# Kernel tuning notes

Hardware: AMD Instinct MI355X
Metric: run time of the kernel (lower is better)

The kernel has to match this reference:

```python
import jax, jax.numpy as jnp
import numpy as np

B, NPTS = 2, 60000
NX, NY = 256, 256
PCR0, PCR1 = -32.0, -32.0
PS0, PS1 = 0.25, 0.25
MAXPP = 32      # max points per pillar
MAXP = 12000    # max pillars
C = 64          # lidar_channels
SENT = NX * NY  # sentinel pillar id (> any valid id)
NEG = -1e9
EPS = 1e-5


def setup_inputs():
    key = jax.random.key(0)
    ks = jax.random.split(key, 16)
    xy = jax.random.uniform(ks[0], (B, NPTS, 2), minval=-34.0, maxval=34.0)
    z = jax.random.uniform(ks[1], (B, NPTS, 1), minval=-3.0, maxval=1.0)
    ir = jax.random.uniform(ks[2], (B, NPTS, 2))
    pts = jnp.concatenate([xy, z, ir], axis=-1).astype(jnp.float32)
    mask = jax.random.uniform(ks[3], (B, NPTS)) < 0.98

    def lin(k, i, o):
        return (jax.random.normal(k, (i, o)) / np.sqrt(i)).astype(jnp.float32)

    inp = {"lidar_points": pts, "lidar_mask": mask,
           "w1": lin(ks[4], 10, 64), "b1": 0.01 * jax.random.normal(ks[5], (64,), jnp.float32),
           "g1": jnp.ones(64, jnp.float32), "be1": jnp.zeros(64, jnp.float32),
           "w2": lin(ks[6], 64, 64), "b2": 0.01 * jax.random.normal(ks[7], (64,), jnp.float32),
           "g2": jnp.ones(64, jnp.float32), "be2": jnp.zeros(64, jnp.float32)}
    for i, n in enumerate(["1", "2", "3"]):
        inp["cw" + n] = (jax.random.normal(ks[8 + i], (64, 64, 3, 3)) / np.sqrt(64 * 9)).astype(jnp.float32)
        inp["cb" + n] = 0.01 * jax.random.normal(ks[11 + i], (64,), jnp.float32)
        inp["cg" + n] = jnp.ones(64, jnp.float32)
        inp["cbe" + n] = jnp.zeros(64, jnp.float32)
    return inp


def bn1d(x, g, b):  # training-mode BN over rows (biased var), matches torch BatchNorm1d forward
    m = x.mean(0)
    v = ((x - m) ** 2).mean(0)
    return (x - m) * jax.lax.rsqrt(v + EPS) * g + b


def bn2d(x, g, b):  # training-mode BN over (N,H,W) per channel
    m = x.mean((0, 2, 3), keepdims=True)
    v = ((x - m) ** 2).mean((0, 2, 3), keepdims=True)
    return (x - m) * jax.lax.rsqrt(v + EPS) * g[None, :, None, None] + b[None, :, None, None]


def conv3(x, w, b):
    y = jax.lax.conv_general_dilated(x, w, (1, 1), 'SAME',
                                     dimension_numbers=('NCHW', 'OIHW', 'NCHW'))
    return y + b[None, :, None, None]


def pillarize(pts, msk):
    """pts: (N,5) xyzir, msk: (N,) bool -> padded pillar tensors (fixed shapes)."""
    n = pts.shape[0]
    ix = jnp.clip(((pts[:, 0] - PCR0) / PS0).astype(jnp.int32), 0, NX - 1)
    iy = jnp.clip(((pts[:, 1] - PCR1) / PS1).astype(jnp.int32), 0, NY - 1)
    pid = jnp.where(msk, iy * NX + ix, SENT)
    # sorted unique ids; keep the first (smallest) MAXP, like torch.unique + truncation
    spid = jnp.sort(pid)
    is_new = jnp.concatenate([jnp.array([True]), spid[1:] != spid[:-1]])
    urank = jnp.cumsum(is_new) - 1
    dest = jnp.where(is_new & (urank < MAXP) & (spid < SENT), urank, MAXP)
    uids = jnp.full((MAXP + 1,), SENT, dtype=pid.dtype).at[dest].set(spid)[:MAXP]  # ascending, SENT-padded
    inv = jnp.clip(jnp.searchsorted(uids, pid), 0, MAXP - 1)
    valid = (uids[inv] == pid) & (pid < SENT)
    # rank of each point within its pillar, in original point order (stable sort)
    seg = jnp.where(valid, inv, MAXP)
    order = jnp.argsort(seg)  # stable
    sseg = seg[order]
    pos = jnp.arange(n)
    first = jnp.concatenate([jnp.array([True]), sseg[1:] != sseg[:-1]])
    start = jax.lax.cummax(jnp.where(first, pos, 0))
    rank = jnp.zeros(n, jnp.int32).at[order].set((pos - start).astype(jnp.int32))
    keep = valid & (rank < MAXPP)  # first MAXPP points per pillar (matches truncation-then-mean)
    seg2 = jnp.where(keep, inv, MAXP)  # dump slot = MAXP
    cnt = jnp.zeros(MAXP + 1, pts.dtype).at[seg2].add(1.0)
    sums = jnp.zeros((MAXP + 1, 3), pts.dtype).at[seg2].add(jnp.where(keep[:, None], pts[:, :3], 0.0))
    mean = sums / jnp.maximum(cnt, 1.0)[:, None]
    ctr = mean[seg2]  # per-point pillar centroid (over kept points)
    gx = PCR0 + ((pid % NX).astype(pts.dtype) + 0.5) * PS0
    gy = PCR1 + ((pid // NX).astype(pts.dtype) + 0.5) * PS1
    aug = jnp.concatenate([pts, pts[:, :3] - ctr, gx[:, None], gy[:, None]], axis=1)  # (N,10)
    rk = jnp.minimum(rank, MAXPP - 1)
    pf = jnp.zeros((MAXP + 1, MAXPP, 10), pts.dtype).at[seg2, rk].set(
        jnp.where(keep[:, None], aug, 0.0))[:MAXP]
    pm = jnp.zeros((MAXP + 1, MAXPP), bool).at[seg2, rk].set(keep)[:MAXP]
    pvalid = uids < SENT
    coords = jnp.where(pvalid[:, None], jnp.stack([uids % NX, uids // NX], axis=-1), 0)
    return pf, pm, coords, pvalid


def pillar_net(pf, pm, w1, b1, g1, be1, w2, b2, g2, be2):
    npil, pp, ci = pf.shape
    x = pf.reshape(npil * pp, ci) @ w1 + b1
    x = jax.nn.relu(bn1d(x, g1, be1))
    x = x @ w2 + b2
    x = jax.nn.relu(bn1d(x, g2, be2))
    x = x.reshape(npil, pp, -1)
    x = jnp.where(pm[:, :, None], x, NEG)
    return x.max(axis=1)  # (npil, C)


def reference(lidar_points, lidar_mask, w1, b1, g1, be1, w2, b2, g2, be2,
              cw1, cb1, cg1, cbe1, cw2, cb2, cg2, cbe2, cw3, cb3, cg3, cbe3):
    pf, pm, coords, pvalid = jax.vmap(pillarize)(lidar_points, lidar_mask)
    # pillar net is applied per batch element in the original loop -> per-sample BN stats
    feat = jax.vmap(lambda a, m: pillar_net(a, m, w1, b1, g1, be1, w2, b2, g2, be2))(pf, pm)
    lin = coords[..., 1] * NX + coords[..., 0]          # (B, MAXP)
    f = jnp.where(pvalid[..., None], feat, 0.0)          # padded pillars contribute nothing
    bev = jax.vmap(lambda l, ff: jnp.zeros((NY * NX, C), ff.dtype).at[l].add(ff))(lin, f)
    bev = bev.reshape(-1, NY, NX, C).transpose(0, 3, 1, 2)  # (B,C,NY,NX)
    x = jax.nn.relu(bn2d(conv3(bev, cw1, cb1), cg1, cbe1))
    x = jax.nn.relu(bn2d(conv3(x, cw2, cb2), cg2, cbe2))
    x = jax.nn.relu(bn2d(conv3(x, cw3, cb3), cg3, cbe3))
    return x
```

## Files before the change

kernel.cpp:

```cpp
#include <hip/hip_runtime.h>

#define NPTS 60000
#define NXG 256
#define NCELL 65536
#define MAXP 12000
#define MAXPP 32
#define NROWS (MAXP*MAXPP)

typedef float f32x32 __attribute__((ext_vector_type(32)));
typedef float f32x4  __attribute__((ext_vector_type(4)));
typedef short s16x8  __attribute__((ext_vector_type(8)));

__device__ __forceinline__ short to_bf16(float f){
  unsigned u = __float_as_uint(f);
  unsigned r = (u + 0x7FFFu + ((u>>16)&1u)) >> 16;
  return (short)r;
}

__global__ void probe_mask(const unsigned* __restrict__ m, int* __restrict__ misc){
  __shared__ int cf32, cbig;
  if (threadIdx.x==0){ cf32=0; cbig=0; }
  __syncthreads();
  int lf=0, lb=0;
  for (int k=0;k<4;k++){
    unsigned x = m[threadIdx.x*4+k];
    if (x==0x3f800000u) lf++;
    else if (x>1u) lb++;
  }
  atomicAdd(&cf32, lf); atomicAdd(&cbig, lb);
  __syncthreads();
  if (threadIdx.x==0){
    int mode=0;
    if (cf32>64) mode=2; else if (cbig>0) mode=1;
    misc[0]=mode;
  }
}

__global__ void compute_pid(const float* __restrict__ pts, const void* __restrict__ maskp,
                            const int* __restrict__ misc, int* __restrict__ pid,
                            int* __restrict__ ccnt){
  int i = blockIdx.x*blockDim.x + threadIdx.x;
  if (i>=NPTS) return;
  int b = blockIdx.y;
  int gi = b*NPTS+i;
  int mode = misc[0];
  bool m;
  if (mode==0)      m = ((const int*)maskp)[gi]!=0;
  else if (mode==1) m = ((const unsigned char*)maskp)[gi]!=0;
  else              m = ((const float*)maskp)[gi]!=0.f;
  int cell = -1;
  if (m){
    float x = pts[(size_t)gi*5+0], y = pts[(size_t)gi*5+1];
    int ix = (int)((x - (-32.0f)) / 0.25f);
    ix = ix<0?0:(ix>255?255:ix);
    int iy = (int)((y - (-32.0f)) / 0.25f);
    iy = iy<0?0:(iy>255?255:iy);
    cell = iy*NXG + ix;
    atomicAdd(&ccnt[b*NCELL+cell], 1);
  }
  pid[gi] = cell;
}

__global__ __launch_bounds__(256) void scan_a(const int* __restrict__ ccnt,
                                              int2* __restrict__ bpart){
  int b = blockIdx.y, blk = blockIdx.x, t = threadIdx.x;
  int4 v = *(const int4*)&ccnt[b*NCELL + blk*1024 + t*4];
  int occ = (v.x>0)+(v.y>0)+(v.z>0)+(v.w>0);
  int cnt = v.x+v.y+v.z+v.w;
  #pragma unroll
  for (int off=32; off>0; off>>=1){
    occ += __shfl_xor(occ, off, 64);
    cnt += __shfl_xor(cnt, off, 64);
  }
  __shared__ int so[4], sc[4];
  int wv = t>>6, lane = t&63;
  if (lane==0){ so[wv]=occ; sc[wv]=cnt; }
  __syncthreads();
  if (t==0) bpart[b*64+blk] = make_int2(so[0]+so[1]+so[2]+so[3], sc[0]+sc[1]+sc[2]+sc[3]);
}

__global__ __launch_bounds__(256) void scan_b(const int* __restrict__ ccnt,
    const int2* __restrict__ bpart,
    int* __restrict__ crank, int* __restrict__ cstart, int* __restrict__ pcell,
    int* __restrict__ misc, int* __restrict__ heavy){
  __shared__ int swo[4], swc[4], sk[4];
  __shared__ int bo_, bc_;
  int b = blockIdx.y, blk = blockIdx.x, t = threadIdx.x;
  int wv = t>>6, lane = t&63;
  if (t < 64){
    int2 p = bpart[b*64+t];
    int po = (t<blk)? p.x : 0;
    int pc = (t<blk)? p.y : 0;
    int to = p.x;
    int tc = p.y;
    #pragma unroll
    for (int off=32; off>0; off>>=1){
      po += __shfl_xor(po, off, 64);
      pc += __shfl_xor(pc, off, 64);
      to += __shfl_xor(to, off, 64);
      tc += __shfl_xor(tc, off, 64);
    }
    if (t==0){
      bo_ = po; bc_ = pc;
      if (blk==0){
        misc[1+b] = (to < MAXP) ? to : MAXP;
        misc[5+b] = tc;
      }
    }
  }
  int4 v = *(const int4*)&ccnt[b*NCELL + blk*1024 + t*4];
  int occ = (v.x>0)+(v.y>0)+(v.z>0)+(v.w>0);
  int cnt = v.x+v.y+v.z+v.w;
  int io = occ, ic = cnt;
  #pragma unroll
  for (int off=1; off<64; off<<=1){
    int ao = __shfl_up(io, off, 64);
    int ac = __shfl_up(ic, off, 64);
    if (lane >= off){ io += ao; ic += ac; }
  }
  if (lane==63){ swo[wv]=io; swc[wv]=ic; }
  __syncthreads();
  int wvo=0, wvc=0;
  #pragma unroll
  for (int w2=0; w2<4; w2++){
    if (w2<wv){ wvo += swo[w2]; wvc += swc[w2]; }
  }
  int eo = bo_ + wvo + io - occ;
  int ec = bc_ + wvc + ic - cnt;
  int kept = 0;
  int cellb = blk*1024 + t*4;
  int vv[4] = {v.x,v.y,v.z,v.w};
  #pragma unroll
  for (int j=0;j<4;j++){
    int c = cellb+j; int val = vv[j];
    if (val>0){
      crank[b*NCELL+c]=eo; cstart[b*NCELL+c]=ec;
      if (eo<MAXP){
        pcell[b*MAXP+eo]=c;
        kept += (val<MAXPP)? val : MAXPP;
        if (val>MAXPP){
          int hi = atomicAdd(&heavy[b],1);
          if (hi<64) heavy[2 + b*64 + hi] = c;
        }
      }
      eo++; ec+=val;
    }
  }
  #pragma unroll
  for (int off=32; off>0; off>>=1) kept += __shfl_xor(kept, off, 64);
  if (lane==0) sk[wv]=kept;
  __syncthreads();
  if (t==0) atomicAdd(&misc[3+b], sk[0]+sk[1]+sk[2]+sk[3]);
}

__global__ void scatter_points(const int* __restrict__ pid, const int* __restrict__ ccnt,
    const int* __restrict__ crank, const int* __restrict__ cstart,
    int* __restrict__ ctmp, int* __restrict__ plist, int* __restrict__ pptr){
  int i = blockIdx.x*blockDim.x + threadIdx.x;
  if (i>=NPTS) return;
  int b = blockIdx.y;
  int gi = b*NPTS+i;
  int cell = pid[gi];
  if (cell<0) return;
  int bc = b*NCELL+cell;
  int pos = cstart[bc] + atomicAdd(&ctmp[bc],1);
  plist[b*NPTS+pos] = i;
  int r = crank[bc];
  if (r>=0 && r<MAXP && ccnt[bc]<=MAXPP) pptr[gi] = r;
}

__global__ void heavy_select(const int* __restrict__ ccnt, const int* __restrict__ crank,
    const int* __restrict__ cstart, const int* __restrict__ plist,
    const int* __restrict__ heavy, int* __restrict__ pptr){
  int b = blockIdx.y;
  int hn = heavy[b]; if (hn>64) hn=64;
  if ((int)blockIdx.x >= hn) return;
  int cell = heavy[2 + b*64 + blockIdx.x];
  int bc = b*NCELL+cell;
  int cnt = ccnt[bc], start = cstart[bc], pr = crank[bc];
  for (int e=threadIdx.x; e<cnt; e+=blockDim.x){
    int pe = plist[b*NPTS+start+e];
    int rank=0;
    for (int k=0;k<cnt;k++) rank += (plist[b*NPTS+start+k] < pe);
    if (rank<MAXPP) pptr[b*NPTS+pe] = pr;
  }
}

__global__ __launch_bounds__(256) void gather_cpts(const float* __restrict__ pts,
    const int* __restrict__ pid, const int* __restrict__ pptr,
    const int* __restrict__ plist, const int* __restrict__ misc,
    float* __restrict__ cpts, float* __restrict__ psum){
  int pos = blockIdx.x*256 + threadIdx.x;
  int b = blockIdx.y;
  if (pos >= misc[5+b]) return;
  int i = plist[b*NPTS+pos];
  int gi = b*NPTS+i;
  const float* qp = &pts[(size_t)gi*5];
  float x=qp[0], y=qp[1], z=qp[2], i1=qp[3], i2=qp[4];
  int cell = pid[gi];
  int rid = pptr[gi];
  float gx = -32.0f + ((float)(cell&255)+0.5f)*0.25f;
  float gy = -32.0f + ((float)(cell>>8)+0.5f)*0.25f;
  float4* cp = (float4*)&cpts[(size_t)(b*NPTS+pos)*8];
  cp[0] = make_float4(x,y,z,i1);
  cp[1] = make_float4(i2,gx,gy,__int_as_float(rid));
  if (rid>=0){
    float* s = &psum[(size_t)(b*MAXP+rid)*4];
    atomicAdd(s+0,x); atomicAdd(s+1,y); atomicAdd(s+2,z); atomicAdd(s+3,1.f);
  }
}

__global__ void centroid_fin(float* __restrict__ psum){
  int i = blockIdx.x*blockDim.x + threadIdx.x;
  if (i>=2*MAXP) return;
  float* s = &psum[(size_t)i*4];
  float inv = 1.0f / fmaxf(s[3],1.0f);
  s[0]*=inv; s[1]*=inv; s[2]*=inv;
}

#define MM_ACC(K,V) { if ((K)<32) m0[(K)&31]+=(V); else if ((K)<64) m1[((K)-32)&31]+=(V); else m2+=(V); }
__global__ __launch_bounds__(256) void moments(const float* __restrict__ cpts,
    const float* __restrict__ psum, const int* __restrict__ misc,
    float* __restrict__ lstat){
  int b = blockIdx.y;
  int n = misc[5+b];
  f32x32 m0, m1; float m2 = 0.f;
  #pragma unroll
  for (int j=0;j<32;j++){ m0[j]=0.f; m1[j]=0.f; }
  for (int pos = blockIdx.x*256+threadIdx.x; pos<n; pos += gridDim.x*256){
    const float4* cp = (const float4*)&cpts[(size_t)(b*NPTS+pos)*8];
    float4 f1 = cp[0], f2 = cp[1];
    int rid = __float_as_int(f2.w);
    if (rid<0) continue;
    float4 mc = *(const float4*)&psum[(size_t)(b*MAXP+rid)*4];
    float aug[10] = {f1.x,f1.y,f1.z,f1.w,f2.x,
                     f1.x-mc.x, f1.y-mc.y, f1.z-mc.z, f2.y, f2.z};
    #pragma unroll
    for (int d=0; d<10; d++){
      #pragma unroll
      for (int e=d; e<10; e++){
        const int k = d*10 - d*(d-1)/2 + (e-d);
        MM_ACC(k, aug[d]*aug[e]);
      }
      const int kl = 55+d;
      MM_ACC(kl, aug[d]);
    }
  }
  int lane = threadIdx.x & 63;
  int rep = ((blockIdx.x*256+threadIdx.x)>>6) & 15;
  float* dst = &lstat[(size_t)(rep*2+b)*65];
  #pragma unroll
  for (int j=0;j<32;j++){
    float v = m0[j];
    #pragma unroll
    for (int off=32; off>0; off>>=1) v += __shfl_xor(v, off, 64);
    if (lane==0) atomicAdd(&dst[j], v);
  }
  #pragma unroll
  for (int j=0;j<32;j++){
    float v = m1[j];
    #pragma unroll
    for (int off=32; off>0; off>>=1) v += __shfl_xor(v, off, 64);
    if (lane==0) atomicAdd(&dst[32+j], v);
  }
  {
    float v = m2;
    #pragma unroll
    for (int off=32; off>0; off>>=1) v += __shfl_xor(v, off, 64);
    if (lane==0) atomicAdd(&dst[64], v);
  }
}

__global__ void stats_fin1(const float* __restrict__ w1, const float* __restrict__ b1,
    const float* __restrict__ g1, const float* __restrict__ be1,
    const float* __restrict__ w2, const float* __restrict__ b2,
    const float* __restrict__ lstat, float* __restrict__ stats,
    const int* __restrict__ misc){
  __shared__ float M[65];
  __shared__ float z0s[64];
  int b = blockIdx.x, c = threadIdx.x;
  for (int e=c; e<65; e+=64){
    float s=0.f;
    for (int r=0;r<16;r++) s += lstat[(size_t)(r*2+b)*65+e];
    M[e]=s;
  }
  __syncthreads();
  float* S = &stats[(size_t)b*512];
  float wcol[10];
  #pragma unroll
  for (int d=0;d<10;d++) wcol[d] = w1[d*64+c];
  float b1c = b1[c];
  float nk = (float)misc[3+b];
  const float N = (float)NROWS;
  float pad = N - nk;
  float lw = 0.f;
  #pragma unroll
  for (int d=0;d<10;d++) lw += M[55+d]*wcol[d];
  float s = nk*b1c + lw;
  float qq = nk*b1c*b1c + 2.f*b1c*lw;
  #pragma unroll
  for (int d=0; d<10; d++){
    #pragma unroll
    for (int e=d; e<10; e++){
      float m = M[d*10 - d*(d-1)/2 + (e-d)];
      qq += ((d==e)?1.f:2.f)*m*wcol[d]*wcol[e];
    }
  }
  float St = s + pad*b1c;
  float Qt = qq + pad*b1c*b1c;
  float mu = St/N;
  float var = fmaxf(Qt/N - mu*mu, 0.f);
  float sc = g1[c]*rsqrtf(var+1e-5f);
  float sh = be1[c]-mu*sc;
  S[256+c]=sc; S[320+c]=sh;
  float z0 = fmaxf(b1c*sc+sh, 0.f);
  z0s[c]=z0;
  __syncthreads();
  float t0 = b2[c];
  for (int i2=0;i2<64;i2++) t0 += z0s[i2]*w2[(size_t)i2*64+c];
  S[128+c]=pad*t0; S[192+c]=pad*t0*t0;
}

__global__ __launch_bounds__(256) void pillar_mlp(const float* __restrict__ cpts,
    const int* __restrict__ pcell, const int* __restrict__ cstart,
    const int* __restrict__ ccnt, const float* __restrict__ psum,
    const int* __restrict__ misc,
    const float* __restrict__ w1, const float* __restrict__ b1,
    const float* __restrict__ w2, const float* __restrict__ b2,
    const float* __restrict__ stats, float* __restrict__ l2stat,
    float* __restrict__ fmx, float* __restrict__ fmn){
  const int lane = threadIdx.x & 63;
  float w1c[10];
  #pragma unroll
  for (int d=0;d<10;d++) w1c[d] = w1[d*64+lane];
  f32x32 w2lo, w2hi;
  #pragma unroll
  for (int c=0;c<32;c++) w2lo[c] = w2[(size_t)c*64+lane];
  #pragma unroll
  for (int c=0;c<32;c++) w2hi[c] = w2[(size_t)(c+32)*64+lane];
  const float b1c = b1[lane], b2c = b2[lane];
  const float sc1_0 = stats[256+lane], sh1_0 = stats[320+lane];
  const float sc1_1 = stats[512+256+lane], sh1_1 = stats[512+320+lane];
  const int npil0 = misc[1], npil1 = misc[2];
  float s2_0=0.f, q2_0=0.f, s2_1=0.f, q2_1=0.f;

  const int wglobal = (blockIdx.x*256 + threadIdx.x) >> 6;
  const int nwaves = (gridDim.x*256) >> 6;
  for (int qq = wglobal; qq < 2*MAXP; qq += nwaves){
    int b = (qq >= MAXP) ? 1 : 0;
    int p = qq - b*MAXP;
    int npil = b ? npil1 : npil0;
    if (p >= npil) continue;
    int cell = pcell[b*MAXP+p];
    int bc = b*NCELL+cell;
    int cnt = ccnt[bc], start = cstart[bc];
    const float* mc = &psum[(size_t)(b*MAXP+p)*4];
    float mx = mc[0], my = mc[1], mz = mc[2];
    float gx = -32.0f + ((float)(cell&255)+0.5f)*0.25f;
    float gy = -32.0f + ((float)(cell>>8)+0.5f)*0.25f;
    float sc1 = b ? sc1_1 : sc1_0;
    float sh1 = b ? sh1_1 : sh1_0;
    float tmax = -1e30f, tmin = 1e30f;
    float s2 = 0.f, q2 = 0.f;
    for (int k=0; k<cnt; k++){
      const float4* cp = (const float4*)&cpts[(size_t)(b*NPTS+start+k)*8];
      float4 f1 = cp[0], f2 = cp[1];
      int rid = __float_as_int(f2.w);
      if (rid != p) continue;
      float x=f1.x, y=f1.y, z=f1.z, i1=f1.w, i2=f2.x;
      float acc = b1c;
      acc = fmaf(x, w1c[0], acc);
      acc = fmaf(y, w1c[1], acc);
      acc = fmaf(z, w1c[2], acc);
      acc = fmaf(i1, w1c[3], acc);
      acc = fmaf(i2, w1c[4], acc);
      acc = fmaf(x-mx, w1c[5], acc);
      acc = fmaf(y-my, w1c[6], acc);
      acc = fmaf(z-mz, w1c[7], acc);
      acc = fmaf(gx, w1c[8], acc);
      acc = fmaf(gy, w1c[9], acc);
      float zz = fmaxf(acc*sc1+sh1, 0.f);
      float t = b2c;
      #pragma unroll
      for (int c=0;c<32;c++){
        float zc = __int_as_float(__builtin_amdgcn_readlane(__float_as_int(zz), c));
        t = fmaf(zc, w2lo[c], t);
      }
      #pragma unroll
      for (int c=0;c<32;c++){
        float zc = __int_as_float(__builtin_amdgcn_readlane(__float_as_int(zz), c+32));
        t = fmaf(zc, w2hi[c], t);
      }
      tmax = fmaxf(tmax, t);
      tmin = fminf(tmin, t);
      s2 += t; q2 += t*t;
    }
    fmx[(size_t)(b*MAXP+p)*64 + lane] = tmax;
    fmn[(size_t)(b*MAXP+p)*64 + lane] = tmin;
    if (b){ s2_1 += s2; q2_1 += q2; } else { s2_0 += s2; q2_0 += q2; }
  }
  int rep = wglobal & 15;
  atomicAdd(&l2stat[((rep*2+0)*2+0)*64+lane], s2_0);
  atomicAdd(&l2stat[((rep*2+0)*2+1)*64+lane], q2_0);
  atomicAdd(&l2stat[((rep*2+1)*2+0)*64+lane], s2_1);
  atomicAdd(&l2stat[((rep*2+1)*2+1)*64+lane], q2_1);
}

__global__ void stats_fin2(const float* __restrict__ g2,const float* __restrict__ be2,
                           const float* __restrict__ l2stat, float* __restrict__ stats){
  int b = blockIdx.x, c = threadIdx.x;
  float* S = &stats[(size_t)b*512];
  float s = S[128+c], q = S[192+c];
  for (int r=0;r<16;r++){
    s += l2stat[((r*2+b)*2+0)*64+c];
    q += l2stat[((r*2+b)*2+1)*64+c];
  }
  const float N = (float)NROWS;
  float m = s/N;
  float v = fmaxf(q/N - m*m, 0.f);
  float sc = g2[c]*rsqrtf(v+1e-5f);
  S[384+c]=sc; S[448+c]=be2[c]-m*sc;
}

__global__ void scatter_bev(const float* __restrict__ fmx, const float* __restrict__ fmn,
                            const int* __restrict__ pcell, const int* __restrict__ misc,
                            const float* __restrict__ stats, short* __restrict__ bevh){
  int tid = blockIdx.x*256+threadIdx.x;
  if (tid >= 2*64*MAXP) return;
  int c = tid & 63;
  int bp = tid >> 6;
  int b = bp / MAXP;
  int p = bp - b*MAXP;
  if (p >= misc[1+b]) return;
  float sc2 = stats[(size_t)b*512+384+c], sh2 = stats[(size_t)b*512+448+c];
  float t = (sc2 >= 0.f) ? fmx[tid] : fmn[tid];
  float v = fmaxf(sc2*t+sh2, 0.f);
  int cell = pcell[b*MAXP+p];
  bevh[((size_t)((b<<16) + cell))*64 + c] = to_bf16(v);
}

__global__ void wcvt3(const float* __restrict__ w0, const float* __restrict__ w1,
                      const float* __restrict__ w2, short* __restrict__ wh){
  int t = blockIdx.x*256 + threadIdx.x;
  if (t >= 3*36864) return;
  int l = t / 36864, r = t - l*36864;
  const float* w = (l==0)? w0 : ((l==1)? w1 : w2);
  int ic = r & 63, oc = (r>>6)&63, tap = r>>12;
  wh[t] = to_bf16(w[(oc*64+ic)*9 + tap]);
}

#define MFMA16(A,B,C) __builtin_amdgcn_mfma_f32_16x16x32_bf16(A,B,C,0,0,0)

__global__ __launch_bounds__(256,2) void conv_mfma(const short* __restrict__ xh,
    const short* __restrict__ wh, const float* __restrict__ bias,
    const float* __restrict__ ibn,
    short* __restrict__ outh, float* __restrict__ outf,
    float* __restrict__ stat){
  __shared__ short sX[18*18*40];
  __shared__ short sW[576*40];
  __shared__ float sBN[128];
  __shared__ float ss[64], sq[64];
  const int tX = blockIdx.x*16, tY = blockIdx.y*16, b = blockIdx.z;
  const int t = threadIdx.x;
  const int lane = t & 63, wv = t >> 6;
  const int colx = lane & 15;
  const int kb = (lane >> 4) * 8;
  if (t < 64){ ss[t]=0.f; sq[t]=0.f; }
  if (ibn && t >= 128 && t < 256) sBN[t-128] = ibn[t-128];

  f32x4 a00={0.f,0.f,0.f,0.f}, a01=a00, a02=a00, a03=a00;
  f32x4 a10=a00, a11=a00, a12=a00, a13=a00;
  f32x4 a20=a00, a21=a00, a22=a00, a23=a00;
  f32x4 a30=a00, a31=a00, a32=a00, a33=a00;

  for (int h=0; h<2; ++h){
    __syncthreads();
    for (int e=t; e<1296; e+=256){
      int px = e>>2, j = e&3;
      int yy = px/18, xx = px - yy*18;
      int gy = tY+yy-1, gx = tX+xx-1;
      uint4 v = make_uint4(0,0,0,0);
      if ((unsigned)gy<256u && (unsigned)gx<256u){
        v = *(const uint4*)&xh[((size_t)((b<<16) + (gy<<8) + gx))*64 + h*32 + j*8];
        if (ibn){
          unsigned arr[4] = {v.x, v.y, v.z, v.w};
          #pragma unroll
          for (int j2=0;j2<4;j2++){
            unsigned wrd = arr[j2];
            int ch = h*32 + j*8 + j2*2;
            float lo = __uint_as_float(wrd<<16);
            float hi = __uint_as_float(wrd & 0xffff0000u);
            lo = fmaxf(lo*sBN[ch]+sBN[64+ch], 0.f);
            hi = fmaxf(hi*sBN[ch+1]+sBN[64+ch+1], 0.f);
            arr[j2] = (unsigned)(unsigned short)to_bf16(lo) |
                      (((unsigned)(unsigned short)to_bf16(hi))<<16);
          }
          v = make_uint4(arr[0],arr[1],arr[2],arr[3]);
        }
      }
      *(uint4*)&sX[px*40 + j*8] = v;
    }
    for (int e=t; e<2304; e+=256){
      int row = e>>2, j = e&3;
      uint4 v = *(const uint4*)&wh[(size_t)row*64 + h*32 + j*8];
      *(uint4*)&sW[row*40 + j*8] = v;
    }
    __syncthreads();
    #pragma unroll
    for (int tap=0; tap<9; ++tap){
      const int dy = tap/3, dx = tap - dy*3;
      s16x8 wA = *(const s16x8*)&sW[(tap*64 +  0 + colx)*40 + kb];
      s16x8 wB = *(const s16x8*)&sW[(tap*64 + 16 + colx)*40 + kb];
      s16x8 wC = *(const s16x8*)&sW[(tap*64 + 32 + colx)*40 + kb];
      s16x8 wD = *(const s16x8*)&sW[(tap*64 + 48 + colx)*40 + kb];
      s16x8 x0 = *(const s16x8*)&sX[((wv*4+0+dy)*18 + colx+dx)*40 + kb];
      s16x8 x1 = *(const s16x8*)&sX[((wv*4+1+dy)*18 + colx+dx)*40 + kb];
      s16x8 x2 = *(const s16x8*)&sX[((wv*4+2+dy)*18 + colx+dx)*40 + kb];
      s16x8 x3 = *(const s16x8*)&sX[((wv*4+3+dy)*18 + colx+dx)*40 + kb];
      a00 = MFMA16(wA,x0,a00); a01 = MFMA16(wA,x1,a01);
      a02 = MFMA16(wA,x2,a02); a03 = MFMA16(wA,x3,a03);
      a10 = MFMA16(wB,x0,a10); a11 = MFMA16(wB,x1,a11);
      a12 = MFMA16(wB,x2,a12); a13 = MFMA16(wB,x3,a13);
      a20 = MFMA16(wC,x0,a20); a21 = MFMA16(wC,x1,a21);
      a22 = MFMA16(wC,x2,a22); a23 = MFMA16(wC,x3,a23);
      a30 = MFMA16(wD,x0,a30); a31 = MFMA16(wD,x1,a31);
      a32 = MFMA16(wD,x2,a32); a33 = MFMA16(wD,x3,a33);
    }
  }
  const int ocl = (lane>>4)*4;
  #define DOG(G, A0,A1,A2,A3) { \
    const int oc0g = G*16 + ocl; \
    float bj0=bias[oc0g], bj1=bias[oc0g+1], bj2=bias[oc0g+2], bj3=bias[oc0g+3]; \
    float v00=A0[0]+bj0, v01=A0[1]+bj1, v02=A0[2]+bj2, v03=A0[3]+bj3; \
    float v10=A1[0]+bj0, v11=A1[1]+bj1, v12=A1[2]+bj2, v13=A1[3]+bj3; \
    float v20=A2[0]+bj0, v21=A2[1]+bj1, v22=A2[2]+bj2, v23=A2[3]+bj3; \
    float v30=A3[0]+bj0, v31=A3[1]+bj1, v32=A3[2]+bj2, v33=A3[3]+bj3; \
    float s0=v00+v10+v20+v30, q0=v00*v00+v10*v10+v20*v20+v30*v30; \
    float s1=v01+v11+v21+v31, q1=v01*v01+v11*v11+v21*v21+v31*v31; \
    float s2=v02+v12+v22+v32, q2=v02*v02+v12*v12+v22*v22+v32*v32; \
    float s3=v03+v13+v23+v33, q3=v03*v03+v13*v13+v23*v23+v33*v33; \
    s0+=__shfl_xor(s0,1,64); s0+=__shfl_xor(s0,2,64); s0+=__shfl_xor(s0,4,64); s0+=__shfl_xor(s0,8,64); \
    q0+=__shfl_xor(q0,1,64); q0+=__shfl_xor(q0,2,64); q0+=__shfl_xor(q0,4,64); q0+=__shfl_xor(q0,8,64); \
    s1+=__shfl_xor(s1,1,64); s1+=__shfl_xor(s1,2,64); s1+=__shfl_xor(s1,4,64); s1+=__shfl_xor(s1,8,64); \
    q1+=__shfl_xor(q1,1,64); q1+=__shfl_xor(q1,2,64); q1+=__shfl_xor(q1,4,64); q1+=__shfl_xor(q1,8,64); \
    s2+=__shfl_xor(s2,1,64); s2+=__shfl_xor(s2,2,64); s2+=__shfl_xor(s2,4,64); s2+=__shfl_xor(s2,8,64); \
    q2+=__shfl_xor(q2,1,64); q2+=__shfl_xor(q2,2,64); q2+=__shfl_xor(q2,4,64); q2+=__shfl_xor(q2,8,64); \
    s3+=__shfl_xor(s3,1,64); s3+=__shfl_xor(s3,2,64); s3+=__shfl_xor(s3,4,64); s3+=__shfl_xor(s3,8,64); \
    q3+=__shfl_xor(q3,1,64); q3+=__shfl_xor(q3,2,64); q3+=__shfl_xor(q3,4,64); q3+=__shfl_xor(q3,8,64); \
    if (colx==0){ \
      atomicAdd(&ss[oc0g],s0);   atomicAdd(&sq[oc0g],q0); \
      atomicAdd(&ss[oc0g+1],s1); atomicAdd(&sq[oc0g+1],q1); \
      atomicAdd(&ss[oc0g+2],s2); atomicAdd(&sq[oc0g+2],q2); \
      atomicAdd(&ss[oc0g+3],s3); atomicAdd(&sq[oc0g+3],q3); \
    } \
    if (outh){ \
      size_t pb = (size_t)((b<<16) + tX + colx); \
      *(short4*)&outh[(pb + ((tY+wv*4+0)<<8))*64 + oc0g] = make_short4(to_bf16(v00),to_bf16(v01),to_bf16(v02),to_bf16(v03)); \
      *(short4*)&outh[(pb + ((tY+wv*4+1)<<8))*64 + oc0g] = make_short4(to_bf16(v10),to_bf16(v11),to_bf16(v12),to_bf16(v13)); \
      *(short4*)&outh[(pb + ((tY+wv*4+2)<<8))*64 + oc0g] = make_short4(to_bf16(v20),to_bf16(v21),to_bf16(v22),to_bf16(v23)); \
      *(short4*)&outh[(pb + ((tY+wv*4+3)<<8))*64 + oc0g] = make_short4(to_bf16(v30),to_bf16(v31),to_bf16(v32),to_bf16(v33)); \
    } else { \
      size_t cb0 = (((size_t)(b*64+oc0g))<<16) + ((tY+wv*4)<<8) + tX + colx; \
      outf[cb0          ] = v00; outf[cb0+(1<<16)      ] = v01; outf[cb0+(2<<16)      ] = v02; outf[cb0+(3<<16)      ] = v03; \
      outf[cb0+256      ] = v10; outf[cb0+(1<<16)+256  ] = v11; outf[cb0+(2<<16)+256  ] = v12; outf[cb0+(3<<16)+256  ] = v13; \
      outf[cb0+512      ] = v20; outf[cb0+(1<<16)+512  ] = v21; outf[cb0+(2<<16)+512  ] = v22; outf[cb0+(3<<16)+512  ] = v23; \
      outf[cb0+768      ] = v30; outf[cb0+(1<<16)+768  ] = v31; outf[cb0+(2<<16)+768  ] = v32; outf[cb0+(3<<16)+768  ] = v33; \
    } \
  }
  DOG(0, a00,a01,a02,a03)
  DOG(1, a10,a11,a12,a13)
  DOG(2, a20,a21,a22,a23)
  DOG(3, a30,a31,a32,a33)
  #undef DOG
  __syncthreads();
  if (t < 64){
    atomicAdd(&stat[t],    ss[t]);
    atomicAdd(&stat[64+t], sq[t]);
  }
}

__global__ void bn_fin(float* __restrict__ bnst, const float* __restrict__ g, const float* __restrict__ be){
  int c = threadIdx.x;
  const float n = 131072.f;
  float m = bnst[c]/n;
  float v = fmaxf(bnst[64+c]/n - m*m, 0.f);
  float sc = g[c]*rsqrtf(v+1e-5f);
  bnst[128+c]=sc; bnst[192+c]=be[c]-m*sc;
}

__global__ __launch_bounds__(256) void bn_apply(float* __restrict__ x, const float* __restrict__ bnst){
  size_t idx = (size_t)blockIdx.x*256 + threadIdx.x;
  size_t stride = (size_t)gridDim.x*256;
  float4* p = (float4*)x;
  for (size_t k=idx; k<2097152ULL; k+=stride){
    int c = (int)((k>>14)&63);
    float sc = bnst[128+c], sh = bnst[192+c];
    float4 v = p[k];
    v.x=fmaxf(v.x*sc+sh,0.f); v.y=fmaxf(v.y*sc+sh,0.f);
    v.z=fmaxf(v.z*sc+sh,0.f); v.w=fmaxf(v.w*sc+sh,0.f);
    p[k]=v;
  }
}

extern "C" void kernel_launch(void* const* d_in, const int* in_sizes, int n_in,
                              void* d_out, int out_size, void* d_ws, size_t ws_size,
                              hipStream_t stream){
  const float* pts  = (const float*)d_in[0];
  const void*  mask = d_in[1];
  const float* w1 = (const float*)d_in[2];
  const float* b1 = (const float*)d_in[3];
  const float* g1 = (const float*)d_in[4];
  const float* be1= (const float*)d_in[5];
  const float* w2 = (const float*)d_in[6];
  const float* b2 = (const float*)d_in[7];
  const float* g2 = (const float*)d_in[8];
  const float* be2= (const float*)d_in[9];
  const float* cw[3]  = {(const float*)d_in[10],(const float*)d_in[14],(const float*)d_in[18]};
  const float* cb[3]  = {(const float*)d_in[11],(const float*)d_in[15],(const float*)d_in[19]};
  const float* cg[3]  = {(const float*)d_in[12],(const float*)d_in[16],(const float*)d_in[20]};
  const float* cbe[3] = {(const float*)d_in[13],(const float*)d_in[17],(const float*)d_in[21]};
  float* out = (float*)d_out;

  char* W = (char*)d_ws;
  size_t off = 0;
  auto A = [&](size_t n){ size_t r = off; off = (off + n + 255) & ~(size_t)255; return r; };
  short*    BIGH  = (short*)   (W + A((size_t)2*NCELL*64*2));
  short*    OUT1H = (short*)   (W + A((size_t)2*NCELL*64*2));
  int*      PID   = (int*)     (W + A((size_t)2*NPTS*4));
  int*      CRANK = (int*)     (W + A((size_t)2*NCELL*4));
  int*      CSTART= (int*)     (W + A((size_t)2*NCELL*4));
  int*      PLIST = (int*)     (W + A((size_t)2*NPTS*4));
  int*      PPTR  = (int*)     (W + A((size_t)2*NPTS*4));
  int*      PCELL = (int*)     (W + A((size_t)2*MAXP*4));
  float*    CPTS  = (float*)   (W + A((size_t)2*NPTS*8*4));
  float*    FMX   = (float*)   (W + A((size_t)2*MAXP*64*4));
  float*    FMN   = (float*)   (W + A((size_t)2*MAXP*64*4));
  short*    WH    = (short*)   (W + A((size_t)3*36864*2));
  int2*     BPART = (int2*)    (W + A((size_t)2*64*8));
  size_t zbeg = off;
  int*      CCNT  = (int*)     (W + A((size_t)2*NCELL*4));
  int*      CTMP  = (int*)     (W + A((size_t)2*NCELL*4));
  float*    PSUM  = (float*)   (W + A((size_t)2*MAXP*16));
  float*    STATS = (float*)   (W + A((size_t)2*512*4));
  float*    LSTAT = (float*)   (W + A((size_t)16*2*65*4));
  float*    L2STAT= (float*)   (W + A((size_t)16*2*2*64*4));
  float*    BNST  = (float*)   (W + A((size_t)3*256*4));
  int*      HEAVY = (int*)     (W + A((size_t)(2+2*64)*4));
  int*      MISC  = (int*)     (W + A(256));
  size_t zend = off;

  hipMemsetAsync(BIGH, 0, (size_t)2*NCELL*64*2, stream);
  hipMemsetAsync(PPTR, 0xFF, (size_t)2*NPTS*4, stream);
  hipMemsetAsync(W+zbeg, 0, zend-zbeg, stream);

  dim3 perPt((NPTS+255)/256, 2);

  probe_mask<<<1,256,0,stream>>>((const unsigned*)mask, MISC);
  compute_pid<<<perPt,256,0,stream>>>(pts, mask, MISC, PID, CCNT);
  wcvt3<<<432,256,0,stream>>>(cw[0], cw[1], cw[2], WH);
  scan_a<<<dim3(64,2),256,0,stream>>>(CCNT, BPART);
  scan_b<<<dim3(64,2),256,0,stream>>>(CCNT, BPART, CRANK, CSTART, PCELL, MISC, HEAVY);
  scatter_points<<<perPt,256,0,stream>>>(PID, CCNT, CRANK, CSTART, CTMP, PLIST, PPTR);
  heavy_select<<<dim3(64,2),64,0,stream>>>(CCNT, CRANK, CSTART, PLIST, HEAVY, PPTR);
  gather_cpts<<<perPt,256,0,stream>>>(pts, PID, PPTR, PLIST, MISC, CPTS, PSUM);
  centroid_fin<<<(2*MAXP+255)/256,256,0,stream>>>(PSUM);
  moments<<<dim3(120,2),256,0,stream>>>(CPTS, PSUM, MISC, LSTAT);
  stats_fin1<<<2,64,0,stream>>>(w1, b1, g1, be1, w2, b2, LSTAT, STATS, MISC);
  pillar_mlp<<<2048,256,0,stream>>>(CPTS, PCELL, CSTART, CCNT, PSUM, MISC,
                                    w1, b1, w2, b2, STATS, L2STAT, FMX, FMN);
  stats_fin2<<<2,64,0,stream>>>(g2, be2, L2STAT, STATS);
  scatter_bev<<<(2*64*MAXP+255)/256,256,0,stream>>>(FMX, FMN, PCELL, MISC, STATS, BIGH);

  conv_mfma<<<dim3(16,16,2),256,0,stream>>>(BIGH, WH, cb[0], nullptr, OUT1H, nullptr, BNST);
  bn_fin<<<1,64,0,stream>>>(BNST, cg[0], cbe[0]);
  conv_mfma<<<dim3(16,16,2),256,0,stream>>>(OUT1H, WH+36864, cb[1], BNST+128, BIGH, nullptr, BNST+256);
  bn_fin<<<1,64,0,stream>>>(BNST+256, cg[1], cbe[1]);
  conv_mfma<<<dim3(16,16,2),256,0,stream>>>(BIGH, WH+2*36864, cb[2], BNST+256+128, nullptr, out, BNST+512);
  bn_fin<<<1,64,0,stream>>>(BNST+512, cg[2], cbe[2]);
  bn_apply<<<2048,256,0,stream>>>(out, BNST+512);
}
```

Measured before the change: 251.3 us.

## Fold mask probe and BN finalize into consumers; read conv weights from global

Merges the mask-format probe into compute_pid, which now also initializes PPTR so that memset is dropped. The BN finalize between convolutions is moved into the next conv's prologue. The conv kernel no longer stages weights in LDS and instead reads them straight from global memory/cache in the tap loop. These changes remove three kernel launches and a memset, and cut LDS use, which may raise occupancy. In exchange, every block redundantly reads the mask probe region and computes BN scale, and weight loads now go through global memory latency inside the MFMA loop.

```diff
diff --git a/kernel.cpp b/kernel.cpp
--- a/kernel.cpp
+++ b/kernel.cpp
@@ -17,33 +17,29 @@
   return (short)r;
 }
 
-__global__ void probe_mask(const unsigned* __restrict__ m, int* __restrict__ misc){
+__global__ void compute_pid(const float* __restrict__ pts, const void* __restrict__ maskp,
+                            int* __restrict__ pid, int* __restrict__ pptr,
+                            int* __restrict__ ccnt){
   __shared__ int cf32, cbig;
   if (threadIdx.x==0){ cf32=0; cbig=0; }
   __syncthreads();
-  int lf=0, lb=0;
-  for (int k=0;k<4;k++){
-    unsigned x = m[threadIdx.x*4+k];
-    if (x==0x3f800000u) lf++;
-    else if (x>1u) lb++;
-  }
-  atomicAdd(&cf32, lf); atomicAdd(&cbig, lb);
-  __syncthreads();
-  if (threadIdx.x==0){
-    int mode=0;
-    if (cf32>64) mode=2; else if (cbig>0) mode=1;
-    misc[0]=mode;
-  }
-}
-
-__global__ void compute_pid(const float* __restrict__ pts, const void* __restrict__ maskp,
-                            const int* __restrict__ misc, int* __restrict__ pid,
-                            int* __restrict__ ccnt){
+  {
+    int lf=0, lb=0;
+    const unsigned* mu = (const unsigned*)maskp;
+    for (int k=0;k<4;k++){
+      unsigned x = mu[threadIdx.x*4+k];
+      if (x==0x3f800000u) lf++;
+      else if (x>1u) lb++;
+    }
+    if (lf) atomicAdd(&cf32, lf);
+    if (lb) atomicAdd(&cbig, lb);
+  }
+  __syncthreads();
+  int mode = (cf32>64) ? 2 : ((cbig>0) ? 1 : 0);
   int i = blockIdx.x*blockDim.x + threadIdx.x;
   if (i>=NPTS) return;
   int b = blockIdx.y;
   int gi = b*NPTS+i;
-  int mode = misc[0];
   bool m;
   if (mode==0)      m = ((const int*)maskp)[gi]!=0;
   else if (mode==1) m = ((const unsigned char*)maskp)[gi]!=0;
@@ -59,6 +55,7 @@
     atomicAdd(&ccnt[b*NCELL+cell], 1);
   }
   pid[gi] = cell;
+  pptr[gi] = -1;
 }
 
 __global__ __launch_bounds__(256) void scan_a(const int* __restrict__ ccnt,
@@ -453,11 +450,10 @@
 
 __global__ __launch_bounds__(256,2) void conv_mfma(const short* __restrict__ xh,
     const short* __restrict__ wh, const float* __restrict__ bias,
-    const float* __restrict__ ibn,
+    const float* __restrict__ pstat, const float* __restrict__ pg, const float* __restrict__ pbe,
     short* __restrict__ outh, float* __restrict__ outf,
     float* __restrict__ stat){
   __shared__ short sX[18*18*40];
-  __shared__ short sW[576*40];
   __shared__ float sBN[128];
   __shared__ float ss[64], sq[64];
   const int tX = blockIdx.x*16, tY = blockIdx.y*16, b = blockIdx.z;
@@ -465,8 +461,16 @@
   const int lane = t & 63, wv = t >> 6;
   const int colx = lane & 15;
   const int kb = (lane >> 4) * 8;
-  if (t < 64){ ss[t]=0.f; sq[t]=0.f; }
-  if (ibn && t >= 128 && t < 256) sBN[t-128] = ibn[t-128];
+  if (t < 64){
+    ss[t]=0.f; sq[t]=0.f;
+    if (pstat){
+      const float n = 131072.f;
+      float m = pstat[t]/n;
+      float v = fmaxf(pstat[64+t]/n - m*m, 0.f);
+      float sc = pg[t]*rsqrtf(v+1e-5f);
+      sBN[t]=sc; sBN[64+t]=pbe[t]-m*sc;
+    }
+  }
 
   f32x4 a00={0.f,0.f,0.f,0.f}, a01=a00, a02=a00, a03=a00;
   f32x4 a10=a00, a11=a00, a12=a00, a13=a00;
@@ -482,7 +486,7 @@
       uint4 v = make_uint4(0,0,0,0);
       if ((unsigned)gy<256u && (unsigned)gx<256u){
         v = *(const uint4*)&xh[((size_t)((b<<16) + (gy<<8) + gx))*64 + h*32 + j*8];
-        if (ibn){
+        if (pstat){
           unsigned arr[4] = {v.x, v.y, v.z, v.w};
           #pragma unroll
           for (int j2=0;j2<4;j2++){
@@ -500,19 +504,15 @@
       }
       *(uint4*)&sX[px*40 + j*8] = v;
     }
-    for (int e=t; e<2304; e+=256){
-      int row = e>>2, j = e&3;
-      uint4 v = *(const uint4*)&wh[(size_t)row*64 + h*32 + j*8];
-      *(uint4*)&sW[row*40 + j*8] = v;
-    }
     __syncthreads();
     #pragma unroll
     for (int tap=0; tap<9; ++tap){
       const int dy = tap/3, dx = tap - dy*3;
-      s16x8 wA = *(const s16x8*)&sW[(tap*64 +  0 + colx)*40 + kb];
-      s16x8 wB = *(const s16x8*)&sW[(tap*64 + 16 + colx)*40 + kb];
-      s16x8 wC = *(const s16x8*)&sW[(tap*64 + 32 + colx)*40 + kb];
-      s16x8 wD = *(const s16x8*)&sW[(tap*64 + 48 + colx)*40 + kb];
+      const short* wb = wh + tap*4096 + colx*64 + h*32 + kb;
+      s16x8 wA = *(const s16x8*)(wb);
+      s16x8 wB = *(const s16x8*)(wb + 1024);
+      s16x8 wC = *(const s16x8*)(wb + 2048);
+      s16x8 wD = *(const s16x8*)(wb + 3072);
       s16x8 x0 = *(const s16x8*)&sX[((wv*4+0+dy)*18 + colx+dx)*40 + kb];
       s16x8 x1 = *(const s16x8*)&sX[((wv*4+1+dy)*18 + colx+dx)*40 + kb];
       s16x8 x2 = *(const s16x8*)&sX[((wv*4+2+dy)*18 + colx+dx)*40 + kb];
@@ -650,13 +650,11 @@
   size_t zend = off;
 
   hipMemsetAsync(BIGH, 0, (size_t)2*NCELL*64*2, stream);
-  hipMemsetAsync(PPTR, 0xFF, (size_t)2*NPTS*4, stream);
   hipMemsetAsync(W+zbeg, 0, zend-zbeg, stream);
 
   dim3 perPt((NPTS+255)/256, 2);
 
-  probe_mask<<<1,256,0,stream>>>((const unsigned*)mask, MISC);
-  compute_pid<<<perPt,256,0,stream>>>(pts, mask, MISC, PID, CCNT);
+  compute_pid<<<perPt,256,0,stream>>>(pts, mask, PID, PPTR, CCNT);
   wcvt3<<<432,256,0,stream>>>(cw[0], cw[1], cw[2], WH);
   scan_a<<<dim3(64,2),256,0,stream>>>(CCNT, BPART);
   scan_b<<<dim3(64,2),256,0,stream>>>(CCNT, BPART, CRANK, CSTART, PCELL, MISC, HEAVY);
@@ -671,11 +669,12 @@
   stats_fin2<<<2,64,0,stream>>>(g2, be2, L2STAT, STATS);
   scatter_bev<<<(2*64*MAXP+255)/256,256,0,stream>>>(FMX, FMN, PCELL, MISC, STATS, BIGH);
 
-  conv_mfma<<<dim3(16,16,2),256,0,stream>>>(BIGH, WH, cb[0], nullptr, OUT1H, nullptr, BNST);
-  bn_fin<<<1,64,0,stream>>>(BNST, cg[0], cbe[0]);
-  conv_mfma<<<dim3(16,16,2),256,0,stream>>>(OUT1H, WH+36864, cb[1], BNST+128, BIGH, nullptr, BNST+256);
-  bn_fin<<<1,64,0,stream>>>(BNST+256, cg[1], cbe[1]);
-  conv_mfma<<<dim3(16,16,2),256,0,stream>>>(BIGH, WH+2*36864, cb[2], BNST+256+128, nullptr, out, BNST+512);
+  conv_mfma<<<dim3(16,16,2),256,0,stream>>>(BIGH, WH, cb[0], nullptr, nullptr, nullptr,
+                                            OUT1H, nullptr, BNST);
+  conv_mfma<<<dim3(16,16,2),256,0,stream>>>(OUT1H, WH+36864, cb[1], BNST, cg[0], cbe[0],
+                                            BIGH, nullptr, BNST+256);
+  conv_mfma<<<dim3(16,16,2),256,0,stream>>>(BIGH, WH+2*36864, cb[2], BNST+256, cg[1], cbe[1],
+                                            nullptr, out, BNST+512);
   bn_fin<<<1,64,0,stream>>>(BNST+512, cg[2], cbe[2]);
   bn_apply<<<2048,256,0,stream>>>(out, BNST+512);
 }
```

After: 262.4 us. 4.4% more time.
